# Optimization experiments

Measured on AMD Instinct MI355X. Metric: run time of the kernel, lower is better.

Reference implementation:

```python
import jax, jax.numpy as jnp
import numpy as np

EMBED = 384
HEADS = 12
DH = EMBED // HEADS  # 32, lucidrains default dim_heads = dim // heads
EPS = 1e-5


def _layernorm(t, g, b):
    mu = jnp.mean(t, axis=-1, keepdims=True)
    var = jnp.mean(jnp.square(t - mu), axis=-1, keepdims=True)
    return (t - mu) * jax.lax.rsqrt(var + EPS) * g + b


def _self_attn(t2, Wq, Wkv, Wo, bo):
    # t2: (N, T, D) -> multi-head self attention (lucidrains SelfAttention)
    N, T, D = t2.shape
    q = t2 @ Wq
    k, v = jnp.split(t2 @ Wkv, 2, axis=-1)
    def split_heads(z):
        return z.reshape(N, T, HEADS, DH).transpose(0, 2, 1, 3)  # (N,H,T,DH)
    q, k, v = map(split_heads, (q, k, v))
    dots = jnp.einsum('nhie,nhje->nhij', q, k) * (DH ** -0.5)
    o = jnp.einsum('nhij,nhje->nhie', jax.nn.softmax(dots, axis=-1), v)
    o = o.transpose(0, 2, 1, 3).reshape(N, T, D)
    return o @ Wo + bo


def _axial(xcl, axis, Wq, Wkv, Wo, bo):
    # xcl channels-last: (b, 3, 16, 16, C); attend along `axis` (1, 2 or 3)
    y = jnp.moveaxis(xcl, axis, -2)
    sh = y.shape
    o = _self_attn(y.reshape(-1, sh[-2], sh[-1]), Wq, Wkv, Wo, bo)
    return jnp.moveaxis(o.reshape(sh), -2, axis)


def setup_inputs() -> dict:
    key = jax.random.key(0)
    ks = jax.random.split(key, 24)
    d, mlp = EMBED, 4 * EMBED
    s = 0.02
    inp = {'x': jax.random.normal(ks[0], (128, 384, 3, 16, 16), jnp.float32)}
    for i in range(3):  # one SelfAttention per axial dim (slice, h, w)
        inp[f'Wq{i}'] = (jax.random.normal(ks[1 + 3 * i], (d, d)) * s).astype(jnp.float32)
        inp[f'Wkv{i}'] = (jax.random.normal(ks[2 + 3 * i], (d, 2 * d)) * s).astype(jnp.float32)
        inp[f'Wo{i}'] = (jax.random.normal(ks[3 + 3 * i], (d, d)) * s).astype(jnp.float32)
        inp[f'bo{i}'] = jnp.zeros((d,), jnp.float32)
    inp['g1'] = jnp.ones((d,), jnp.float32)
    inp['be1'] = jnp.zeros((d,), jnp.float32)
    inp['W1m'] = (jax.random.normal(ks[10], (d, mlp)) * s).astype(jnp.float32)
    inp['b1m'] = jnp.zeros((mlp,), jnp.float32)
    inp['W2m'] = (jax.random.normal(ks[11], (mlp, d)) * s).astype(jnp.float32)
    inp['b2m'] = jnp.zeros((d,), jnp.float32)
    inp['g2'] = jnp.ones((d,), jnp.float32)
    inp['be2'] = jnp.zeros((d,), jnp.float32)
    return inp


def reference(x, Wq0, Wkv0, Wo0, bo0, Wq1, Wkv1, Wo1, bo1, Wq2, Wkv2, Wo2, bo2,
              g1, be1, W1m, b1m, W2m, b2m, g2, be2):
    # x: (B, C=384, 3, 16, 16); dropout is identity in eval mode
    xcl = jnp.moveaxis(x, 1, -1)  # (B, 3, 16, 16, C)
    attn = (_axial(xcl, 1, Wq0, Wkv0, Wo0, bo0)
            + _axial(xcl, 2, Wq1, Wkv1, Wo1, bo1)
            + _axial(xcl, 3, Wq2, Wkv2, Wo2, bo2))  # sum_axial_out=True
    xcl = xcl + attn  # residual
    B = xcl.shape[0]
    t = xcl.reshape(B, 3 * 16 * 16, EMBED)  # == x.flatten(2).transpose(1,2)
    t = _layernorm(t, g1, be1)
    m = jax.nn.gelu(t @ W1m + b1m, approximate=False) @ W2m + b2m
    t = _layernorm(t + m, g2, be2)
    return jnp.moveaxis(t.reshape(B, 3, 16, 16, EMBED), -1, 1)
```

## Files before the change

kernel.cpp:

```cpp
#include <hip/hip_runtime.h>

typedef unsigned short u16;
typedef __bf16 bf16;
typedef bf16  bf16x4 __attribute__((ext_vector_type(4)));
typedef bf16  bf16x8 __attribute__((ext_vector_type(8)));
typedef float f32x4  __attribute__((ext_vector_type(4)));

__device__ __forceinline__ u16  f2b(float v) { return __builtin_bit_cast(u16, (bf16)v); }
__device__ __forceinline__ float b2f(u16 b)  { return (float)__builtin_bit_cast(bf16, b); }

__global__ void probe_dtype(const float* xf, int* flag) {
    __shared__ int cnt[256];
    const int tid = threadIdx.x;
    int good = 0;
#pragma unroll
    for (int i = 0; i < 4; ++i) {
        const float a = fabsf(xf[tid * 4 + i]);
        if (a > 9.5e-7f && a < 1.0e6f) good++;
    }
    cnt[tid] = good;
    __syncthreads();
    if (tid == 0) { int s = 0; for (int i = 0; i < 256; ++i) s += cnt[i]; *flag = (s > 512) ? 1 : 0; }
}

__global__ void cvt_vec(const void* in, bf16* out, int n, const int* flag) {
    const int f32 = *flag;
    for (int i = blockIdx.x * 256 + threadIdx.x; i < n; i += gridDim.x * 256)
        out[i] = f32 ? (bf16)(((const float*)in)[i])
                     : __builtin_bit_cast(bf16, ((const u16*)in)[i]);
}

__global__ void zfill(bf16* p, int n) {
    for (int i = blockIdx.x * 256 + threadIdx.x; i < n; i += gridDim.x * 256) p[i] = (bf16)0.f;
}

__global__ void transpose_cvt(const void* in, u16* out, size_t base_off, int R, int C, const int* flag) {
    __shared__ u16 tile[32][34];
    const int f32 = *flag;
    const int c0 = blockIdx.x * 32, r0 = blockIdx.y * 32;
    const size_t bi = base_off + (size_t)blockIdx.z * R * C;
    const size_t bo = (size_t)blockIdx.z * R * C;
    const int tx = threadIdx.x, ty = threadIdx.y;
#pragma unroll
    for (int i = 0; i < 4; ++i) {
        const size_t idx = bi + (size_t)(r0 + ty + i * 8) * C + c0 + tx;
        tile[ty + i * 8][tx] = f32 ? f2b(((const float*)in)[idx]) : ((const u16*)in)[idx];
    }
    __syncthreads();
#pragma unroll
    for (int i = 0; i < 4; ++i)
        out[bo + (size_t)(c0 + ty + i * 8) * R + r0 + tx] = tile[tx][ty + i * 8];
}

__global__ void transpose_out(const u16* in, void* out, size_t base_off, int R, int C, const int* flag) {
    __shared__ u16 tile[32][34];
    const int f32 = *flag;
    const int c0 = blockIdx.x * 32, r0 = blockIdx.y * 32;
    const size_t bi = (size_t)blockIdx.z * R * C;
    const size_t bo = base_off + (size_t)blockIdx.z * R * C;
    const int tx = threadIdx.x, ty = threadIdx.y;
#pragma unroll
    for (int i = 0; i < 4; ++i)
        tile[ty + i * 8][tx] = in[bi + (size_t)(r0 + ty + i * 8) * C + c0 + tx];
    __syncthreads();
#pragma unroll
    for (int i = 0; i < 4; ++i) {
        const size_t o = bo + (size_t)(c0 + ty + i * 8) * R + r0 + tx;
        const u16 v = tile[tx][ty + i * 8];
        if (f32) ((float*)out)[o] = b2f(v); else ((u16*)out)[o] = v;
    }
}

__device__ __forceinline__ void gld_lds16(const bf16* g, bf16* l) {
    __builtin_amdgcn_global_load_lds((__attribute__((address_space(1))) void*)g,
                                     (__attribute__((address_space(3))) void*)l,
                                     16, 0, 0);
}

template<int MODE>
__global__ __launch_bounds__(512)
void gemm256(const bf16* __restrict__ A, const bf16* __restrict__ BT,
             bf16* C, const bf16* __restrict__ bias, int M, int N, int K)
{
    __shared__ __align__(16) bf16 sm[65536];
    const int tid = threadIdx.x;

    const int gx = gridDim.x, gy = gridDim.y;
    int lin = blockIdx.y * gx + blockIdx.x;
    const int nwg = gx * gy;
    const int q = nwg >> 3, r8 = nwg & 7;
    const int xcd = lin & 7, idx = lin >> 3;
    lin = (xcd < r8 ? xcd * (q + 1) : r8 * (q + 1) + (xcd - r8) * q) + idx;
    const int bm0 = (lin / gy) * 256;
    const int bn0 = (lin % gy) * 256;

    const int lane = tid & 63, wid = tid >> 6;
    const int wr = wid >> 2, wc = wid & 3;
    const int fr = lane & 15, fg = lane >> 4;
    const int arow = tid >> 3;
    const int scol = ((tid & 7) ^ (arow & 7)) << 3;

    const bf16* Ab = A  + (size_t)(bm0 + arow) * K + scol;
    const bf16* Bb = BT + (size_t)(bn0 + arow) * K + scol;

    bf16* const lA0 = sm;
    bf16* const lA1 = sm + 16384;
    bf16* const lB0 = sm + 32768;
    bf16* const lB1 = sm + 49152;

    f32x4 acc[8][4] = {};
    const int NT = K >> 6;

#pragma unroll
    for (int i = 0; i < 4; ++i) gld_lds16(Ab + (size_t)i * 64 * K, lA0 + i * 4096 + tid * 8);
#pragma unroll
    for (int i = 0; i < 4; ++i) gld_lds16(Bb + (size_t)i * 64 * K, lB0 + i * 4096 + tid * 8);
    __syncthreads();

    const int sw = fr & 7;
    for (int t = 0; t < NT; ++t) {
        if (t + 1 < NT) {
            const int k0 = (t + 1) << 6;
            bf16* la = ((t + 1) & 1) ? lA1 : lA0;
            bf16* lb = ((t + 1) & 1) ? lB1 : lB0;
#pragma unroll
            for (int i = 0; i < 4; ++i) gld_lds16(Ab + k0 + (size_t)i * 64 * K, la + i * 4096 + tid * 8);
#pragma unroll
            for (int i = 0; i < 4; ++i) gld_lds16(Bb + k0 + (size_t)i * 64 * K, lb + i * 4096 + tid * 8);
        }
        const bf16* la = (t & 1) ? lA1 : lA0;
        const bf16* lb = (t & 1) ? lB1 : lB0;
#pragma unroll
        for (int kk = 0; kk < 2; ++kk) {
            const int so = ((((kk << 2) + fg) ^ sw) << 3);
            bf16x8 bfv[4];
#pragma unroll
            for (int n = 0; n < 4; ++n)
                bfv[n] = *(const bf16x8*)&lb[(wc * 64 + n * 16 + fr) * 64 + so];
#pragma unroll
            for (int m = 0; m < 8; ++m) {
                const bf16x8 af = *(const bf16x8*)&la[(wr * 128 + m * 16 + fr) * 64 + so];
#pragma unroll
                for (int n = 0; n < 4; ++n)
                    acc[m][n] = __builtin_amdgcn_mfma_f32_16x16x32_bf16(af, bfv[n], acc[m][n], 0, 0, 0);
            }
        }
        __syncthreads();
    }

#pragma unroll
    for (int n = 0; n < 4; ++n) {
        const int col = wc * 64 + n * 16 + fr;
        const float bv = (MODE == 2) ? (float)bias[bn0 + col] : 0.f;
#pragma unroll
        for (int m = 0; m < 8; ++m) {
            const int row0 = wr * 128 + m * 16 + fg * 4;
#pragma unroll
            for (int r = 0; r < 4; ++r) {
                float v = acc[m][n][r];
                if (MODE == 2) { v += bv; v = 0.5f * v * (1.f + erff(v * 0.70710678118654752f)); }
                sm[(row0 + r) * 256 + col] = (bf16)v;
            }
        }
    }
    __syncthreads();
#pragma unroll
    for (int it = 0; it < 16; ++it) {
        const int chunk = it * 512 + tid;
        const int row = chunk >> 5, c8 = (chunk & 31) << 3;
        *(bf16x8*)&C[(size_t)(bm0 + row) * N + bn0 + c8] = *(const bf16x8*)&sm[row * 256 + c8];
    }
}

template<int MODE>
__global__ __launch_bounds__(256)
void gemm_bt(const bf16* __restrict__ A, const bf16* __restrict__ BT,
             bf16* C, const bf16* __restrict__ bias,
             const bf16* add, int M, int N, int K)
{
    __shared__ __align__(16) bf16 sm[4][8192];
    const int tid = threadIdx.x;

    const int gx = gridDim.x, gy = gridDim.y;
    int lin = blockIdx.y * gx + blockIdx.x;
    const int nwg = gx * gy;
    const int q = nwg >> 3, r8 = nwg & 7;
    const int xcd = lin & 7, idx = lin >> 3;
    lin = (xcd < r8 ? xcd * (q + 1) : r8 * (q + 1) + (xcd - r8) * q) + idx;
    const int bm0 = (lin / gy) * 128;
    const int bn0 = (lin % gy) * 128;

    const int lane = tid & 63, wid = tid >> 6;
    const int wr = wid >> 1, wc = wid & 1;
    const int fr = lane & 15, fg = lane >> 4;
    const int arow = tid >> 3;
    const int scol = ((tid & 7) ^ (arow & 7)) << 3;

    const bf16* Ab = A  + (size_t)(bm0 + arow) * K + scol;
    const bf16* Bb = BT + (size_t)(bn0 + arow) * K + scol;

    f32x4 acc[4][4] = {};
    const int NT = K >> 6;
    {
        bf16* la = sm[0];
        bf16* lb = sm[1];
#pragma unroll
        for (int i = 0; i < 4; ++i) gld_lds16(Ab + (size_t)i * 32 * K, &la[i * 2048 + tid * 8]);
#pragma unroll
        for (int i = 0; i < 4; ++i) gld_lds16(Bb + (size_t)i * 32 * K, &lb[i * 2048 + tid * 8]);
    }
    __syncthreads();

    const int sw = fr & 7;
    for (int t = 0; t < NT; ++t) {
        if (t + 1 < NT) {
            const int k0 = (t + 1) << 6;
            bf16* la = sm[2 * ((t + 1) & 1)];
            bf16* lb = sm[2 * ((t + 1) & 1) + 1];
#pragma unroll
            for (int i = 0; i < 4; ++i) gld_lds16(Ab + k0 + (size_t)i * 32 * K, &la[i * 2048 + tid * 8]);
#pragma unroll
            for (int i = 0; i < 4; ++i) gld_lds16(Bb + k0 + (size_t)i * 32 * K, &lb[i * 2048 + tid * 8]);
        }
        const bf16* la = sm[2 * (t & 1)];
        const bf16* lb = sm[2 * (t & 1) + 1];
#pragma unroll
        for (int kk = 0; kk < 2; ++kk) {
            bf16x8 af[4], bfv[4];
#pragma unroll
            for (int m = 0; m < 4; ++m)
                af[m] = *(const bf16x8*)&la[(wr * 64 + m * 16 + fr) * 64 + ((((kk << 2) + fg) ^ sw) << 3)];
#pragma unroll
            for (int n = 0; n < 4; ++n)
                bfv[n] = *(const bf16x8*)&lb[(wc * 64 + n * 16 + fr) * 64 + ((((kk << 2) + fg) ^ sw) << 3)];
#pragma unroll
            for (int m = 0; m < 4; ++m)
#pragma unroll
                for (int n = 0; n < 4; ++n)
                    acc[m][n] = __builtin_amdgcn_mfma_f32_16x16x32_bf16(af[m], bfv[n], acc[m][n], 0, 0, 0);
        }
        __syncthreads();
    }

    float* lc = (float*)sm;
#pragma unroll
    for (int n = 0; n < 4; ++n) {
        const int col = wc * 64 + n * 16 + fr;
#pragma unroll
        for (int m = 0; m < 4; ++m) {
            const int row0 = wr * 64 + m * 16 + fg * 4;
#pragma unroll
            for (int r2 = 0; r2 < 4; ++r2)
                lc[(row0 + r2) * 128 + col] = acc[m][n][r2];
        }
    }
    __syncthreads();
    const f32x4* lc4 = (const f32x4*)sm;
#pragma unroll
    for (int i = 0; i < 16; ++i) {
        const int chunk = i * 256 + tid;
        const int row = chunk >> 5, cb = (chunk & 31) * 4;
        const size_t goff = (size_t)(bm0 + row) * N + bn0 + cb;
        const f32x4 v = lc4[chunk];
        bf16x4 o;
        if (MODE == 1) {
            const bf16x4 bv = *(const bf16x4*)&bias[bn0 + cb];
            const bf16x4 av = *(const bf16x4*)&add[goff];
#pragma unroll
            for (int e = 0; e < 4; ++e) o[e] = (bf16)(v[e] + (float)bv[e] + (float)av[e]);
        } else {
#pragma unroll
            for (int e = 0; e < 4; ++e) o[e] = (bf16)v[e];
        }
        *(bf16x4*)&C[goff] = o;
    }
}

__global__ __launch_bounds__(256)
void attn16(const bf16* __restrict__ QKV, bf16* __restrict__ O, int tstride, int lastmul, int qs)
{
    const int lane = threadIdx.x & 63;
    const int gw   = (blockIdx.x * 256 + threadIdx.x) >> 6;
    const int head = gw % 12;
    const int seq  = gw / 12;
    const int b    = seq / 48, r2 = seq % 48;
    const int s    = r2 >> 4, last = r2 & 15;
    const int tbase = b * 768 + s * 256 + last * lastmul;
    const int fr = lane & 15, fg = lane >> 4;

    const size_t rowQ = (size_t)(tbase + fr * tstride) * qs + head * 32 + fg * 8;
    const bf16x8 kf = *(const bf16x8*)(QKV + rowQ + 384);
    const bf16x8 qf = *(const bf16x8*)(QKV + rowQ);
    const f32x4 z = {0.f, 0.f, 0.f, 0.f};
    f32x4 S = __builtin_amdgcn_mfma_f32_16x16x32_bf16(kf, qf, z, 0, 0, 0);

    const float sc = 0.17677669529663687f;
    float mx = fmaxf(fmaxf(S[0], S[1]), fmaxf(S[2], S[3]));
    mx = fmaxf(mx, __shfl_xor(mx, 16));
    mx = fmaxf(mx, __shfl_xor(mx, 32));
    float p[4], sum = 0.f;
#pragma unroll
    for (int r = 0; r < 4; ++r) { p[r] = __expf((S[r] - mx) * sc); sum += p[r]; }
    sum += __shfl_xor(sum, 16);
    sum += __shfl_xor(sum, 32);
    const float inv = 1.f / sum;

    bf16x8 pa;
#pragma unroll
    for (int j = 0; j < 8; ++j) {
        const int srcg = 2 * fg + (j >> 2);
        const float v = __shfl(p[j & 3], fr + 16 * (srcg & 3));
        pa[j] = (bf16)(fg < 2 ? v * inv : 0.f);
    }

#pragma unroll
    for (int t = 0; t < 2; ++t) {
        bf16x8 vf;
#pragma unroll
        for (int j = 0; j < 8; ++j) {
            const int key = fg * 8 + j;
            vf[j] = (fg < 2)
                ? QKV[(size_t)(tbase + key * tstride) * qs + 768 + head * 32 + fr + 16 * t]
                : (bf16)0.f;
        }
        f32x4 o = __builtin_amdgcn_mfma_f32_16x16x32_bf16(pa, vf, z, 0, 0, 0);
#pragma unroll
        for (int r = 0; r < 4; ++r)
            O[(size_t)(tbase + (fg * 4 + r) * tstride) * 384 + head * 32 + fr + 16 * t] = (bf16)o[r];
    }
}

__global__ __launch_bounds__(256)
void attn3(const bf16* __restrict__ QKV, bf16* __restrict__ O, int qs)
{
    const int t    = blockIdx.x * 256 + threadIdx.x;
    const int head = t % 12;
    const int seq  = t / 12;
    const int b    = seq >> 8, hw = seq & 255;
    const size_t base  = (size_t)(b * 768 + hw) * qs + head * 32;
    const size_t tstep = (size_t)256 * qs;

    float s[3][3] = {};
#pragma unroll
    for (int c = 0; c < 4; ++c) {
        bf16x8 q[3], k[3];
#pragma unroll
        for (int i = 0; i < 3; ++i) {
            q[i] = *(const bf16x8*)(QKV + base + i * tstep + c * 8);
            k[i] = *(const bf16x8*)(QKV + base + i * tstep + 384 + c * 8);
        }
#pragma unroll
        for (int i = 0; i < 3; ++i)
#pragma unroll
            for (int j = 0; j < 3; ++j) {
                float a = 0.f;
#pragma unroll
                for (int e = 0; e < 8; ++e) a += (float)q[i][e] * (float)k[j][e];
                s[i][j] += a;
            }
    }
    const float sc = 0.17677669529663687f;
    float p[3][3];
#pragma unroll
    for (int i = 0; i < 3; ++i) {
        const float mx = fmaxf(s[i][0], fmaxf(s[i][1], s[i][2]));
        float sum = 0.f;
#pragma unroll
        for (int j = 0; j < 3; ++j) { p[i][j] = __expf((s[i][j] - mx) * sc); sum += p[i][j]; }
        const float inv = 1.f / sum;
#pragma unroll
        for (int j = 0; j < 3; ++j) p[i][j] *= inv;
    }
    const size_t obase = (size_t)(b * 768 + hw) * 384 + head * 32;
#pragma unroll
    for (int c = 0; c < 4; ++c) {
        bf16x8 v[3];
#pragma unroll
        for (int j = 0; j < 3; ++j) v[j] = *(const bf16x8*)(QKV + base + j * tstep + 768 + c * 8);
#pragma unroll
        for (int i = 0; i < 3; ++i) {
            bf16x8 ov;
#pragma unroll
            for (int e = 0; e < 8; ++e)
                ov[e] = (bf16)(p[i][0] * (float)v[0][e] + p[i][1] * (float)v[1][e] + p[i][2] * (float)v[2][e]);
            *(bf16x8*)(O + obase + (size_t)i * 256 * 384 + c * 8) = ov;
        }
    }
}

__global__ __launch_bounds__(256)
void ln_kernel(const bf16* __restrict__ in, bf16* __restrict__ out,
               const bf16* __restrict__ g, const bf16* __restrict__ be, int ntok)
{
    const int w    = (blockIdx.x * 256 + threadIdx.x) >> 6;
    const int lane = threadIdx.x & 63;
    if (w >= ntok) return;
    const bf16* row = in + (size_t)w * 384;
    float x[6], sum = 0.f;
#pragma unroll
    for (int i = 0; i < 6; ++i) { x[i] = (float)row[lane + i * 64]; sum += x[i]; }
#pragma unroll
    for (int o = 32; o >= 1; o >>= 1) sum += __shfl_xor(sum, o);
    const float mu = sum * (1.f / 384.f);
    float vs = 0.f;
#pragma unroll
    for (int i = 0; i < 6; ++i) { const float d = x[i] - mu; vs += d * d; }
#pragma unroll
    for (int o = 32; o >= 1; o >>= 1) vs += __shfl_xor(vs, o);
    const float rstd = rsqrtf(vs * (1.f / 384.f) + 1e-5f);
    bf16* orow = out + (size_t)w * 384;
#pragma unroll
    for (int i = 0; i < 6; ++i)
        orow[lane + i * 64] = (bf16)((x[i] - mu) * rstd * (float)g[lane + i * 64] + (float)be[lane + i * 64]);
}

extern "C" void kernel_launch(void* const* d_in, const int* in_sizes, int n_in,
                              void* d_out, int out_size, void* d_ws, size_t ws_size,
                              hipStream_t stream)
{
    const void* x = d_in[0];
    const void *Wq[3], *Wkv[3], *Wo[3], *bo[3];
    for (int i = 0; i < 3; ++i) {
        Wq[i]  = d_in[1 + 4 * i];
        Wkv[i] = d_in[2 + 4 * i];
        Wo[i]  = d_in[3 + 4 * i];
        bo[i]  = d_in[4 + 4 * i];
    }
    const void* g1  = d_in[13];
    const void* be1 = d_in[14];
    const void* W1m = d_in[15];
    const void* b1m = d_in[16];
    const void* W2m = d_in[17];
    const void* b2m = d_in[18];
    const void* g2  = d_in[19];
    const void* be2 = d_in[20];

    char* ws = (char*)d_ws;
    bf16* qkvT  = (bf16*)(ws);
    bf16* woT[3];
    for (int i = 0; i < 3; ++i) woT[i] = (bf16*)(ws + 2752512ull + (size_t)i * 294912ull);
    bf16* w1mT = (bf16*)(ws + 3637248ull);
    bf16* w2mT = (bf16*)(ws + 4816896ull);
    bf16* vbo[3]; bf16 *vg1, *vbe1, *vg2, *vbe2, *vb1m, *vb2m;
    {
        char* vp = ws + 5996544ull;
        vbo[0] = (bf16*)(vp);            vbo[1] = (bf16*)(vp + 768);  vbo[2] = (bf16*)(vp + 1536);
        vg1  = (bf16*)(vp + 2304);       vbe1 = (bf16*)(vp + 3072);
        vg2  = (bf16*)(vp + 3840);       vbe2 = (bf16*)(vp + 4608);
        vb1m = (bf16*)(vp + 5376);       vb2m = (bf16*)(vp + 8448);
    }
    int* dflag = (int*)(ws + 6006784ull);
    const size_t WB = 6553600ull;

    int NB = 32;
    while (NB > 1) {
        size_t need = WB + (size_t)NB * 768 * (4 * 384 + 3584) * 2;
        if (need <= ws_size) break;
        NB >>= 1;
    }
    const int Tc = NB * 768;
    const size_t tokB = (size_t)Tc * 384 * 2;
    bf16* Xc   = (bf16*)(ws + WB);
    bf16* ABc  = (bf16*)(ws + WB + tokB);
    bf16* T1c  = (bf16*)(ws + WB + 2 * tokB);
    bf16* ATOc = (bf16*)(ws + WB + 3 * tokB);
    bf16* BIGc = (bf16*)(ws + WB + 4 * tokB);

    probe_dtype<<<1, 256, 0, stream>>>((const float*)x, dflag);
    for (int i = 0; i < 3; ++i)
        cvt_vec<<<2, 256, 0, stream>>>(bo[i], vbo[i], 384, dflag);
    cvt_vec<<<2, 256, 0, stream>>>(g1,  vg1,  384,  dflag);
    cvt_vec<<<2, 256, 0, stream>>>(be1, vbe1, 384,  dflag);
    cvt_vec<<<2, 256, 0, stream>>>(g2,  vg2,  384,  dflag);
    cvt_vec<<<2, 256, 0, stream>>>(be2, vbe2, 384,  dflag);
    cvt_vec<<<6, 256, 0, stream>>>(b1m, vb1m, 1536, dflag);
    cvt_vec<<<2, 256, 0, stream>>>(b2m, vb2m, 384,  dflag);
    zfill<<<48, 256, 0, stream>>>(qkvT + 3456 * 384, 128 * 384);

    const dim3 tb(32, 8);
    for (int i = 0; i < 3; ++i) {
        transpose_cvt<<<dim3(12, 12, 1), tb, 0, stream>>>(Wq[i],  (u16*)(qkvT + (size_t)(i * 1152) * 384),        0, 384, 384, dflag);
        transpose_cvt<<<dim3(24, 12, 1), tb, 0, stream>>>(Wkv[i], (u16*)(qkvT + (size_t)(i * 1152 + 384) * 384),  0, 384, 768, dflag);
        transpose_cvt<<<dim3(12, 12, 1), tb, 0, stream>>>(Wo[i],  (u16*)woT[i],                                    0, 384, 384, dflag);
    }
    transpose_cvt<<<dim3(48, 12, 1), tb, 0, stream>>>(W1m, (u16*)w1mT, 0, 384, 1536, dflag);
    transpose_cvt<<<dim3(12, 48, 1), tb, 0, stream>>>(W2m, (u16*)w2mT, 0, 1536, 384, dflag);

    for (int b0 = 0; b0 < 128; b0 += NB) {
        const size_t xoff = (size_t)b0 * 384 * 768;
        transpose_cvt<<<dim3(24, 12, NB), tb, 0, stream>>>(x, (u16*)Xc, xoff, 384, 768, dflag);

        gemm256<0><<<dim3(Tc / 256, 14), 512, 0, stream>>>(Xc, qkvT, BIGc, nullptr, Tc, 3584, 384);

        for (int i = 0; i < 3; ++i) {
            const bf16* qkv_i = BIGc + (size_t)i * 1152;
            if (i == 0)      attn3 <<<NB * 12,  256, 0, stream>>>(qkv_i, ATOc, 3584);
            else if (i == 1) attn16<<<NB * 144, 256, 0, stream>>>(qkv_i, ATOc, 16, 1, 3584);
            else             attn16<<<NB * 144, 256, 0, stream>>>(qkv_i, ATOc, 1, 16, 3584);
            gemm_bt<1><<<dim3(Tc / 128, 3), 256, 0, stream>>>(ATOc, woT[i], ABc, vbo[i], (i == 0) ? Xc : ABc, Tc, 384, 384);
        }
        ln_kernel<<<Tc / 4, 256, 0, stream>>>(ABc, T1c, vg1, vbe1, Tc);
        gemm256<2><<<dim3(Tc / 256, 6), 512, 0, stream>>>(T1c, w1mT, BIGc, vb1m, Tc, 1536, 384);
        gemm_bt<1><<<dim3(Tc / 128, 3), 256, 0, stream>>>(BIGc, w2mT, ABc, vb2m, T1c, Tc, 384, 1536);
        ln_kernel<<<Tc / 4, 256, 0, stream>>>(ABc, Xc, vg2, vbe2, Tc);
        transpose_out<<<dim3(12, 24, NB), tb, 0, stream>>>((const u16*)Xc, d_out, xoff, 768, 384, dflag);
    }
}
```

Baseline: 1.674 ms.

## Fuse three axial output projections into one K=1152 GEMM with summed bias

The three axial attention outputs are now written side by side into a 1152-wide buffer, and the three Wo matrices are stacked into one transposed weight. A single GEMM with K=1152 replaces three K=384 GEMMs that each re-read and re-wrote the accumulator, and the three output biases are pre-summed into one vector. This removes two GEMM launches and their extra residual read/write traffic. In exchange it needs a larger attention-output workspace, so the chunk size NB drops from 32 to 16, which doubles the number of per-chunk loop iterations.

```diff
diff --git a/kernel.cpp b/kernel.cpp
--- a/kernel.cpp
+++ b/kernel.cpp
@@ -30,16 +30,26 @@
                      : __builtin_bit_cast(bf16, ((const u16*)in)[i]);
 }
 
+__global__ void sum3_vec(const void* a, const void* b, const void* c, bf16* out, int n, const int* flag) {
+    const int f32 = *flag;
+    for (int i = blockIdx.x * 256 + threadIdx.x; i < n; i += gridDim.x * 256) {
+        float va, vb, vc;
+        if (f32) { va = ((const float*)a)[i]; vb = ((const float*)b)[i]; vc = ((const float*)c)[i]; }
+        else { va = b2f(((const u16*)a)[i]); vb = b2f(((const u16*)b)[i]); vc = b2f(((const u16*)c)[i]); }
+        out[i] = (bf16)(va + vb + vc);
+    }
+}
+
 __global__ void zfill(bf16* p, int n) {
     for (int i = blockIdx.x * 256 + threadIdx.x; i < n; i += gridDim.x * 256) p[i] = (bf16)0.f;
 }
 
-__global__ void transpose_cvt(const void* in, u16* out, size_t base_off, int R, int C, const int* flag) {
+__global__ void transpose_cvt(const void* in, u16* out, size_t base_off, int R, int C, int ostride, const int* flag) {
     __shared__ u16 tile[32][34];
     const int f32 = *flag;
     const int c0 = blockIdx.x * 32, r0 = blockIdx.y * 32;
     const size_t bi = base_off + (size_t)blockIdx.z * R * C;
-    const size_t bo = (size_t)blockIdx.z * R * C;
+    const size_t bo = (size_t)blockIdx.z * C * ostride;
     const int tx = threadIdx.x, ty = threadIdx.y;
 #pragma unroll
     for (int i = 0; i < 4; ++i) {
@@ -49,7 +59,7 @@
     __syncthreads();
 #pragma unroll
     for (int i = 0; i < 4; ++i)
-        out[bo + (size_t)(c0 + ty + i * 8) * R + r0 + tx] = tile[tx][ty + i * 8];
+        out[bo + (size_t)(c0 + ty + i * 8) * ostride + r0 + tx] = tile[tx][ty + i * 8];
 }
 
 __global__ void transpose_out(const u16* in, void* out, size_t base_off, int R, int C, const int* flag) {
@@ -277,7 +287,7 @@
 }
 
 __global__ __launch_bounds__(256)
-void attn16(const bf16* __restrict__ QKV, bf16* __restrict__ O, int tstride, int lastmul, int qs)
+void attn16(const bf16* __restrict__ QKV, bf16* __restrict__ O, int tstride, int lastmul, int qs, int os)
 {
     const int lane = threadIdx.x & 63;
     const int gw   = (blockIdx.x * 256 + threadIdx.x) >> 6;
@@ -326,12 +336,12 @@
         f32x4 o = __builtin_amdgcn_mfma_f32_16x16x32_bf16(pa, vf, z, 0, 0, 0);
 #pragma unroll
         for (int r = 0; r < 4; ++r)
-            O[(size_t)(tbase + (fg * 4 + r) * tstride) * 384 + head * 32 + fr + 16 * t] = (bf16)o[r];
+            O[(size_t)(tbase + (fg * 4 + r) * tstride) * os + head * 32 + fr + 16 * t] = (bf16)o[r];
     }
 }
 
 __global__ __launch_bounds__(256)
-void attn3(const bf16* __restrict__ QKV, bf16* __restrict__ O, int qs)
+void attn3(const bf16* __restrict__ QKV, bf16* __restrict__ O, int qs, int os)
 {
     const int t    = blockIdx.x * 256 + threadIdx.x;
     const int head = t % 12;
@@ -371,7 +381,7 @@
 #pragma unroll
         for (int j = 0; j < 3; ++j) p[i][j] *= inv;
     }
-    const size_t obase = (size_t)(b * 768 + hw) * 384 + head * 32;
+    const size_t obase = (size_t)(b * 768 + hw) * os + head * 32;
 #pragma unroll
     for (int c = 0; c < 4; ++c) {
         bf16x8 v[3];
@@ -383,7 +393,7 @@
 #pragma unroll
             for (int e = 0; e < 8; ++e)
                 ov[e] = (bf16)(p[i][0] * (float)v[0][e] + p[i][1] * (float)v[1][e] + p[i][2] * (float)v[2][e]);
-            *(bf16x8*)(O + obase + (size_t)i * 256 * 384 + c * 8) = ov;
+            *(bf16x8*)(O + obase + (size_t)i * 256 * os + c * 8) = ov;
         }
     }
 }
@@ -436,25 +446,24 @@
     const void* be2 = d_in[20];
 
     char* ws = (char*)d_ws;
-    bf16* qkvT  = (bf16*)(ws);
-    bf16* woT[3];
-    for (int i = 0; i < 3; ++i) woT[i] = (bf16*)(ws + 2752512ull + (size_t)i * 294912ull);
+    bf16* qkvT = (bf16*)(ws);
+    bf16* woTf = (bf16*)(ws + 2752512ull);
     bf16* w1mT = (bf16*)(ws + 3637248ull);
     bf16* w2mT = (bf16*)(ws + 4816896ull);
-    bf16* vbo[3]; bf16 *vg1, *vbe1, *vg2, *vbe2, *vb1m, *vb2m;
+    bf16 *vboS, *vg1, *vbe1, *vg2, *vbe2, *vb1m, *vb2m;
     {
         char* vp = ws + 5996544ull;
-        vbo[0] = (bf16*)(vp);            vbo[1] = (bf16*)(vp + 768);  vbo[2] = (bf16*)(vp + 1536);
-        vg1  = (bf16*)(vp + 2304);       vbe1 = (bf16*)(vp + 3072);
-        vg2  = (bf16*)(vp + 3840);       vbe2 = (bf16*)(vp + 4608);
-        vb1m = (bf16*)(vp + 5376);       vb2m = (bf16*)(vp + 8448);
-    }
-    int* dflag = (int*)(ws + 6006784ull);
+        vboS = (bf16*)(vp);
+        vg1  = (bf16*)(vp + 768);        vbe1 = (bf16*)(vp + 1536);
+        vg2  = (bf16*)(vp + 2304);       vbe2 = (bf16*)(vp + 3072);
+        vb1m = (bf16*)(vp + 3840);       vb2m = (bf16*)(vp + 6912);
+    }
+    int* dflag = (int*)(ws + 6007296ull);
     const size_t WB = 6553600ull;
 
-    int NB = 32;
+    int NB = 16;
     while (NB > 1) {
-        size_t need = WB + (size_t)NB * 768 * (4 * 384 + 3584) * 2;
+        size_t need = WB + (size_t)NB * 768 * (6 * 384 + 3584) * 2;
         if (need <= ws_size) break;
         NB >>= 1;
     }
@@ -464,11 +473,10 @@
     bf16* ABc  = (bf16*)(ws + WB + tokB);
     bf16* T1c  = (bf16*)(ws + WB + 2 * tokB);
     bf16* ATOc = (bf16*)(ws + WB + 3 * tokB);
-    bf16* BIGc = (bf16*)(ws + WB + 4 * tokB);
+    bf16* BIGc = (bf16*)(ws + WB + 6 * tokB);
 
     probe_dtype<<<1, 256, 0, stream>>>((const float*)x, dflag);
-    for (int i = 0; i < 3; ++i)
-        cvt_vec<<<2, 256, 0, stream>>>(bo[i], vbo[i], 384, dflag);
+    sum3_vec<<<2, 256, 0, stream>>>(bo[0], bo[1], bo[2], vboS, 384, dflag);
     cvt_vec<<<2, 256, 0, stream>>>(g1,  vg1,  384,  dflag);
     cvt_vec<<<2, 256, 0, stream>>>(be1, vbe1, 384,  dflag);
     cvt_vec<<<2, 256, 0, stream>>>(g2,  vg2,  384,  dflag);
@@ -479,26 +487,25 @@
 
     const dim3 tb(32, 8);
     for (int i = 0; i < 3; ++i) {
-        transpose_cvt<<<dim3(12, 12, 1), tb, 0, stream>>>(Wq[i],  (u16*)(qkvT + (size_t)(i * 1152) * 384),        0, 384, 384, dflag);
-        transpose_cvt<<<dim3(24, 12, 1), tb, 0, stream>>>(Wkv[i], (u16*)(qkvT + (size_t)(i * 1152 + 384) * 384),  0, 384, 768, dflag);
-        transpose_cvt<<<dim3(12, 12, 1), tb, 0, stream>>>(Wo[i],  (u16*)woT[i],                                    0, 384, 384, dflag);
-    }
-    transpose_cvt<<<dim3(48, 12, 1), tb, 0, stream>>>(W1m, (u16*)w1mT, 0, 384, 1536, dflag);
-    transpose_cvt<<<dim3(12, 48, 1), tb, 0, stream>>>(W2m, (u16*)w2mT, 0, 1536, 384, dflag);
+        transpose_cvt<<<dim3(12, 12, 1), tb, 0, stream>>>(Wq[i],  (u16*)(qkvT + (size_t)(i * 1152) * 384),       0, 384, 384, 384, dflag);
+        transpose_cvt<<<dim3(24, 12, 1), tb, 0, stream>>>(Wkv[i], (u16*)(qkvT + (size_t)(i * 1152 + 384) * 384), 0, 384, 768, 384, dflag);
+        transpose_cvt<<<dim3(12, 12, 1), tb, 0, stream>>>(Wo[i],  (u16*)(woTf + i * 384),                        0, 384, 384, 1152, dflag);
+    }
+    transpose_cvt<<<dim3(48, 12, 1), tb, 0, stream>>>(W1m, (u16*)w1mT, 0, 384, 1536, 384,  dflag);
+    transpose_cvt<<<dim3(12, 48, 1), tb, 0, stream>>>(W2m, (u16*)w2mT, 0, 1536, 384, 1536, dflag);
 
     for (int b0 = 0; b0 < 128; b0 += NB) {
         const size_t xoff = (size_t)b0 * 384 * 768;
-        transpose_cvt<<<dim3(24, 12, NB), tb, 0, stream>>>(x, (u16*)Xc, xoff, 384, 768, dflag);
+        transpose_cvt<<<dim3(24, 12, NB), tb, 0, stream>>>(x, (u16*)Xc, xoff, 384, 768, 384, dflag);
 
         gemm256<0><<<dim3(Tc / 256, 14), 512, 0, stream>>>(Xc, qkvT, BIGc, nullptr, Tc, 3584, 384);
 
-        for (int i = 0; i < 3; ++i) {
-            const bf16* qkv_i = BIGc + (size_t)i * 1152;
-            if (i == 0)      attn3 <<<NB * 12,  256, 0, stream>>>(qkv_i, ATOc, 3584);
-            else if (i == 1) attn16<<<NB * 144, 256, 0, stream>>>(qkv_i, ATOc, 16, 1, 3584);
-            else             attn16<<<NB * 144, 256, 0, stream>>>(qkv_i, ATOc, 1, 16, 3584);
-            gemm_bt<1><<<dim3(Tc / 128, 3), 256, 0, stream>>>(ATOc, woT[i], ABc, vbo[i], (i == 0) ? Xc : ABc, Tc, 384, 384);
-        }
+        attn3 <<<NB * 12,  256, 0, stream>>>(BIGc,            ATOc,          3584, 1152);
+        attn16<<<NB * 144, 256, 0, stream>>>(BIGc + 1152,     ATOc + 384, 16, 1, 3584, 1152);
+        attn16<<<NB * 144, 256, 0, stream>>>(BIGc + 2304,     ATOc + 768, 1, 16, 3584, 1152);
+
+        gemm_bt<1><<<dim3(Tc / 128, 3), 256, 0, stream>>>(ATOc, woTf, ABc, vboS, Xc, Tc, 384, 1152);
+
         ln_kernel<<<Tc / 4, 256, 0, stream>>>(ABc, T1c, vg1, vbe1, Tc);
         gemm256<2><<<dim3(Tc / 256, 6), 512, 0, stream>>>(T1c, w1mT, BIGc, vb1m, Tc, 1536, 384);
         gemm_bt<1><<<dim3(Tc / 128, 3), 256, 0, stream>>>(BIGc, w2mT, ABc, vb2m, T1c, Tc, 384, 1536);
```

Result: slower. 1.768 ms (+5.6%).
